# Optimization experiments

Hardware: AMD Instinct MI355X
Metric: run time of the kernel (lower is better)

Reference implementation:

```python
import jax, jax.numpy as jnp
import numpy as np

N_EMBD = 1024
N_HEAD = 16
HEAD_DIM = N_EMBD // N_HEAD


def setup_inputs() -> dict:
    key = jax.random.key(0)
    ks = jax.random.split(key, 9)
    B, T, C = 4, 2048, N_EMBD
    s = 1.0 / np.sqrt(C)
    return {
        "x": jax.random.normal(ks[0], (B, T, C), dtype=jnp.float32),
        "Wq": jax.random.normal(ks[1], (C, C), dtype=jnp.float32) * s,
        "bq": jnp.zeros((C,), dtype=jnp.float32),
        "Wk": jax.random.normal(ks[2], (C, C), dtype=jnp.float32) * s,
        "bk": jnp.zeros((C,), dtype=jnp.float32),
        "Wv": jax.random.normal(ks[3], (C, C), dtype=jnp.float32) * s,
        "bv": jnp.zeros((C,), dtype=jnp.float32),
        "Wo": jax.random.normal(ks[4], (C, C), dtype=jnp.float32) * s,
        "bo": jnp.zeros((C,), dtype=jnp.float32),
    }


def reference(x, Wq, bq, Wk, bk, Wv, bv, Wo, bo):
    B, T, C = x.shape
    H, D = N_HEAD, HEAD_DIM
    # torch Linear: y = x @ W.T + b ; here W stored as (in, out) so y = x @ W + b
    q = (x @ Wq + bq).reshape(B, T, H, D).transpose(0, 2, 1, 3)  # [B,H,T,D]
    k = (x @ Wk + bk).reshape(B, T, H, D).transpose(0, 2, 1, 3)
    v = (x @ Wv + bv).reshape(B, T, H, D).transpose(0, 2, 1, 3)
    scores = jnp.einsum('bhqd,bhkd->bhqk', q, k) / jnp.sqrt(jnp.float32(D))
    causal = jnp.tril(jnp.ones((T, T), dtype=bool))  # [T,T]
    scores = jnp.where(causal[None, None, :, :], scores, -jnp.inf)
    weights = jax.nn.softmax(scores, axis=-1)
    # dropout disabled (eval mode / deterministic reference)
    out = jnp.einsum('bhqk,bhkd->bhqd', weights, v)  # [B,H,T,D]
    out = out.transpose(0, 2, 1, 3).reshape(B, T, C)
    return out @ Wo + bo
```

## Files before the change

kernel.cpp:

```cpp
#include <hip/hip_runtime.h>
#include <stdint.h>
#include <stddef.h>

#define NB 4
#define NT 2048
#define NC 1024
#define NH 16
#define ND 64
#define NM (NB*NT)
#define KVB 64

typedef __bf16 bf16_t;
typedef __attribute__((ext_vector_type(8)))  __bf16 bf16x8;
typedef __attribute__((ext_vector_type(4)))  __bf16 bf16x4;
typedef __attribute__((ext_vector_type(2)))  __bf16 bf16x2;
typedef __attribute__((ext_vector_type(4)))  float  f32x4;
typedef __attribute__((ext_vector_type(16))) float  f32x16;
typedef __attribute__((ext_vector_type(4)))  unsigned int u32x4;

#define QK_SCALE_LOG2E 0.18033688011112042f

__device__ __forceinline__ f32x4 mfma_bf16(bf16x8 a, bf16x8 b, f32x4 c) {
  return __builtin_amdgcn_mfma_f32_16x16x32_bf16(a, b, c, 0, 0, 0);
}
__device__ __forceinline__ f32x16 mfma32(bf16x8 a, bf16x8 b, f32x16 c) {
  return __builtin_amdgcn_mfma_f32_32x32x16_bf16(a, b, c, 0, 0, 0);
}

__device__ __forceinline__ void gld_lds16(const void* g, void* l) {
  __builtin_amdgcn_global_load_lds(
      (const __attribute__((address_space(1))) void*)g,
      (__attribute__((address_space(3))) void*)l, 16, 0, 0);
}

__device__ __forceinline__ unsigned int pack_bf16(float a, float b) {
  bf16x2 t; t[0] = (bf16_t)a; t[1] = (bf16_t)b;
  return __builtin_bit_cast(unsigned int, t);
}

#if __has_builtin(__builtin_amdgcn_permlane32_swap)
typedef __attribute__((ext_vector_type(2))) unsigned int u32x2;
__device__ __forceinline__ void plswap(unsigned int &a, unsigned int &b) {
  u32x2 r = __builtin_amdgcn_permlane32_swap(a, b, false, false);
  a = r[0]; b = r[1];
}
#else
__device__ __forceinline__ void plswap(unsigned int &a, unsigned int &b) {
  asm volatile("s_nop 1\n\tv_permlane32_swap_b32 %0, %1\n\ts_nop 1"
               : "+v"(a), "+v"(b));
}
#endif

__global__ __launch_bounds__(256) void cast_x_kernel(const float* __restrict__ x,
                                                     bf16_t* __restrict__ xb, int n4) {
  const int stride = gridDim.x * blockDim.x;
  for (int i = blockIdx.x * blockDim.x + threadIdx.x; i < n4; i += stride) {
    float4 v = reinterpret_cast<const float4*>(x)[i];
    bf16x4 o;
    o[0] = (bf16_t)v.x; o[1] = (bf16_t)v.y; o[2] = (bf16_t)v.z; o[3] = (bf16_t)v.w;
    reinterpret_cast<bf16x4*>(xb)[i] = o;
  }
}

__global__ __launch_bounds__(256) void transpose_cast_kernel(const float* __restrict__ W,
                                                             bf16_t* __restrict__ WT) {
  __shared__ float tile[32][33];
  const int t = threadIdx.x;
  const int tx = t & 31, ty = t >> 5;
  const int k0 = (blockIdx.x & 31) << 5;
  const int n0 = (blockIdx.x >> 5) << 5;
#pragma unroll
  for (int i = 0; i < 4; ++i)
    tile[ty + 8*i][tx] = W[(size_t)(k0 + ty + 8*i)*NC + n0 + tx];
  __syncthreads();
#pragma unroll
  for (int i = 0; i < 4; ++i)
    WT[(size_t)(n0 + ty + 8*i)*NC + k0 + tx] = (bf16_t)tile[tx][ty + 8*i];
}

template<int MODE>
__global__ __launch_bounds__(256) void gemm_bt_kernel(
    const bf16_t* __restrict__ A, const bf16_t* __restrict__ BT,
    int M, int N, int K,
    bf16_t* __restrict__ qo, bf16_t* __restrict__ ko, bf16_t* __restrict__ vo,
    const float* __restrict__ b0, const float* __restrict__ b1, const float* __restrict__ b2,
    float* __restrict__ outp, const float* __restrict__ bo)
{
  const int lane = threadIdx.x & 63;
  const int wv = threadIdx.x >> 6;
  const int wr = wv >> 1, wc = wv & 1;
  const int l15 = lane & 15, lg = lane >> 4;
  const int nbn = N >> 7;
  const int bm = blockIdx.x / nbn, bn = blockIdx.x % nbn;
  const int m0 = bm << 7, n0 = bn << 7;

  __shared__ char smem[32768];
  char* As = smem;
  char* Bs = smem + 16384;

  f32x4 acc[4][4] = {};

  const int nkt = K >> 6;
  for (int kt = 0; kt < nkt; ++kt) {
    const int k0 = kt << 6;
    __syncthreads();
#pragma unroll
    for (int i = 0; i < 4; ++i) {
      const int seg = i*4 + wv;
      const int lin = seg*64 + lane;
      const int row = lin >> 3;
      const int ch  = (lin & 7) ^ (row & 7);
      gld_lds16(A  + (size_t)(m0 + row)*K + k0 + (ch << 3), As + seg*1024);
      gld_lds16(BT + (size_t)(n0 + row)*K + k0 + (ch << 3), Bs + seg*1024);
    }
    __syncthreads();
#pragma unroll
    for (int ks = 0; ks < 2; ++ks) {
      bf16x8 af[4], bfr[4];
#pragma unroll
      for (int fr = 0; fr < 4; ++fr) {
        const int row = wr*64 + fr*16 + l15;
        const int ch  = (ks*4 + lg) ^ (row & 7);
        af[fr] = *reinterpret_cast<const bf16x8*>(As + row*128 + ch*16);
      }
#pragma unroll
      for (int fc = 0; fc < 4; ++fc) {
        const int row = wc*64 + fc*16 + l15;
        const int ch  = (ks*4 + lg) ^ (row & 7);
        bfr[fc] = *reinterpret_cast<const bf16x8*>(Bs + row*128 + ch*16);
      }
#pragma unroll
      for (int fr = 0; fr < 4; ++fr)
#pragma unroll
        for (int fc = 0; fc < 4; ++fc)
          acc[fr][fc] = mfma_bf16(af[fr], bfr[fc], acc[fr][fc]);
    }
  }

#pragma unroll
  for (int fr = 0; fr < 4; ++fr) {
#pragma unroll
    for (int fc = 0; fc < 4; ++fc) {
      const int mrow0 = m0 + wr*64 + fr*16 + (lg << 2);
      const int ncol  = n0 + wc*64 + fc*16 + l15;
      if (MODE == 0) {
        const int mat = ncol >> 10, c = ncol & 1023;
        const int h = c >> 6, d = c & 63;
        if (mat == 2) {
          const float bias = b2[c];
          bf16x4 ov;
#pragma unroll
          for (int r = 0; r < 4; ++r) ov[r] = (bf16_t)(acc[fr][fc][r] + bias);
          const int bb = mrow0 >> 11, tt = mrow0 & (NT - 1);
          *reinterpret_cast<bf16x4*>(vo + ((((size_t)bb*NH + h)*ND + d)*NT) + tt) = ov;
        } else {
          bf16_t* dst = (mat == 0) ? qo : ko;
          const float* bptr = (mat == 0) ? b0 : b1;
          const float bias = bptr[c];
          const float scl = (mat == 0) ? QK_SCALE_LOG2E : 1.0f;
#pragma unroll
          for (int r = 0; r < 4; ++r) {
            const int mm = mrow0 + r;
            const int bb = mm >> 11, tt = mm & (NT - 1);
            dst[((((size_t)bb*NH + h)*NT + tt) << 6) + d] =
                (bf16_t)((acc[fr][fc][r] + bias) * scl);
          }
        }
      } else {
        const float bias = bo[ncol];
#pragma unroll
        for (int r = 0; r < 4; ++r)
          outp[(size_t)(mrow0 + r)*N + ncol] = acc[fr][fc][r] + bias;
      }
    }
  }
}

__global__ __launch_bounds__(512, 2) void attn_kernel(
    const bf16_t* __restrict__ q, const bf16_t* __restrict__ k, const bf16_t* __restrict__ vt,
    bf16_t* __restrict__ o)
{
  const int tid  = threadIdx.x;
  const int lane = tid & 63;
  const int wv   = tid >> 6;
  const int l31  = lane & 31, h = lane >> 5;

  const int tile = 7 - (blockIdx.x >> 6);
  const int bh   = blockIdx.x & 63;
  const int bb = bh >> 4, hh = bh & 15;
  const int q0 = tile << 8;

  __shared__ char smem[4*8192];
  char* const ks0 = smem;
  char* const ks1 = smem + 8192;
  char* const vs0 = smem + 16384;
  char* const vs1 = smem + 24576;

  const size_t base = (size_t)bh * (NT * ND);
  const bf16_t* Kg = k  + base;
  const bf16_t* Vg = vt + base;

  const int q0w = q0 + wv*32;
  const int qg  = q0w + l31;

  const int srow = tid >> 3;
  const int sch  = (tid & 7) ^ (srow & 7);
  const int offk = srow*ND + (sch << 3);
  const int offv = srow*NT + (sch << 3);
  const int segb = wv << 10;

  gld_lds16(Kg + offk, ks0 + segb);
  gld_lds16(Vg + offv, vs0 + segb);

  bf16x8 qf[4];
  {
    const bf16_t* Qg = q + base + (size_t)qg*ND + 8*h;
#pragma unroll
    for (int ds = 0; ds < 4; ++ds)
      qf[ds] = *reinterpret_cast<const bf16x8*>(Qg + 16*ds);
  }

  bf16x8 ones8;
#pragma unroll
  for (int jj = 0; jj < 8; ++jj) ones8[jj] = (bf16_t)1.0f;

  f32x16 oc[2] = {};
  f32x16 lacc = {};

  const int nkv = 4*(tile + 1);

  for (int j = 0; j < nkv; ++j) {
    const int kt0 = j << 6;
    const bool cur1 = (j & 1) != 0;
    char* const Kc = cur1 ? ks1 : ks0;
    char* const Vc = cur1 ? vs1 : vs0;

    asm volatile("s_waitcnt vmcnt(0)" ::: "memory");
    __builtin_amdgcn_s_barrier();
    __builtin_amdgcn_sched_barrier(0);

    if (j + 1 < nkv) {
      char* const Kn = cur1 ? ks0 : ks1;
      char* const Vn = cur1 ? vs0 : vs1;
      gld_lds16(Kg + (j + 1)*(KVB*ND) + offk, Kn + segb);
      gld_lds16(Vg + (j + 1)*KVB      + offv, Vn + segb);
      __builtin_amdgcn_sched_barrier(0);
    }

    if (kt0 <= q0w + 31) {
      f32x16 st[2] = {};
      __builtin_amdgcn_s_setprio(1);
#pragma unroll
      for (int ds = 0; ds < 4; ++ds) {
#pragma unroll
        for (int kt = 0; kt < 2; ++kt) {
          const int row = kt*32 + l31;
          const int cl  = (2*ds + h) ^ (row & 7);
          const bf16x8 kfr = *reinterpret_cast<const bf16x8*>(Kc + row*128 + cl*16);
          st[kt] = mfma32(kfr, qf[ds], st[kt]);
        }
      }
      __builtin_amdgcn_s_setprio(0);

      if (kt0 + KVB - 1 > q0w) {
        const int qrel = qg - kt0 - 4*h;
#pragma unroll
        for (int kt = 0; kt < 2; ++kt)
#pragma unroll
          for (int r = 0; r < 16; ++r) {
            const int kc = (r & 3) + 8*(r >> 2) + 32*kt;
            st[kt][r] = (kc > qrel) ? 0.0f : exp2f(st[kt][r]);
          }
      } else {
#pragma unroll
        for (int kt = 0; kt < 2; ++kt)
#pragma unroll
          for (int r = 0; r < 16; ++r)
            st[kt][r] = exp2f(st[kt][r]);
      }

#pragma unroll
      for (int kt = 0; kt < 2; ++kt) {
#pragma unroll
        for (int g = 0; g < 2; ++g) {
          unsigned int wa = pack_bf16(st[kt][8*g + 0], st[kt][8*g + 1]);
          unsigned int wb = pack_bf16(st[kt][8*g + 2], st[kt][8*g + 3]);
          unsigned int wc = pack_bf16(st[kt][8*g + 4], st[kt][8*g + 5]);
          unsigned int wd = pack_bf16(st[kt][8*g + 6], st[kt][8*g + 7]);
          plswap(wa, wc);
          plswap(wb, wd);
          u32x4 pb; pb[0] = wa; pb[1] = wb; pb[2] = wc; pb[3] = wd;
          const bf16x8 pf = __builtin_bit_cast(bf16x8, pb);
          const int kg = 2*kt + g;
          __builtin_amdgcn_s_setprio(1);
          lacc = mfma32(ones8, pf, lacc);
#pragma unroll
          for (int da = 0; da < 2; ++da) {
            const int row = 32*da + l31;
            const int cl  = (2*kg + h) ^ (row & 7);
            const bf16x8 vf = *reinterpret_cast<const bf16x8*>(Vc + row*128 + cl*16);
            oc[da] = mfma32(vf, pf, oc[da]);
          }
          __builtin_amdgcn_s_setprio(0);
        }
      }
    }
  }

  const float rl = 1.0f / lacc[0];
  bf16_t* orow = o + ((size_t)bb*NT + qg)*NC + hh*ND;
#pragma unroll
  for (int da = 0; da < 2; ++da) {
#pragma unroll
    for (int u = 0; u < 4; ++u) {
      bf16x4 ov;
#pragma unroll
      for (int jj = 0; jj < 4; ++jj) ov[jj] = (bf16_t)(oc[da][4*u + jj] * rl);
      *reinterpret_cast<bf16x4*>(orow + 32*da + 8*u + 4*h) = ov;
    }
  }
}

extern "C" void kernel_launch(void* const* d_in, const int* in_sizes, int n_in,
                              void* d_out, int out_size, void* d_ws, size_t ws_size,
                              hipStream_t stream) {
  (void)in_sizes; (void)n_in; (void)out_size;
  const float* x  = (const float*)d_in[0];
  const float* Wq = (const float*)d_in[1];
  const float* bq = (const float*)d_in[2];
  const float* Wk = (const float*)d_in[3];
  const float* bk = (const float*)d_in[4];
  const float* Wv = (const float*)d_in[5];
  const float* bv = (const float*)d_in[6];
  const float* Wo = (const float*)d_in[7];
  const float* bo = (const float*)d_in[8];
  float* out = (float*)d_out;

  const size_t off_xb    = 0;
  const size_t off_wqkvT = 16777216;
  const size_t off_woT   = 23068672;
  const size_t off_q     = 25165824;
  const size_t off_k     = 41943040;
  const size_t off_v     = 58720256;
  const size_t off_attn  = 75497472;
  const size_t need      = 92274688;
  if (ws_size < need) return;

  char* ws = (char*)d_ws;
  bf16_t* xb    = (bf16_t*)(ws + off_xb);
  bf16_t* wqkvT = (bf16_t*)(ws + off_wqkvT);
  bf16_t* woT   = (bf16_t*)(ws + off_woT);
  bf16_t* qb    = (bf16_t*)(ws + off_q);
  bf16_t* kb    = (bf16_t*)(ws + off_k);
  bf16_t* vtb   = (bf16_t*)(ws + off_v);
  bf16_t* attnb = (bf16_t*)(ws + off_attn);

  cast_x_kernel<<<dim3(2048), dim3(256), 0, stream>>>(x, xb, NM*NC/4);
  transpose_cast_kernel<<<dim3(1024), dim3(256), 0, stream>>>(Wq, wqkvT);
  transpose_cast_kernel<<<dim3(1024), dim3(256), 0, stream>>>(Wk, wqkvT + 1048576);
  transpose_cast_kernel<<<dim3(1024), dim3(256), 0, stream>>>(Wv, wqkvT + 2097152);
  transpose_cast_kernel<<<dim3(1024), dim3(256), 0, stream>>>(Wo, woT);

  gemm_bt_kernel<0><<<dim3(64*24), dim3(256), 0, stream>>>(
      xb, wqkvT, NM, 3*NC, NC, qb, kb, vtb, bq, bk, bv, nullptr, nullptr);

  attn_kernel<<<dim3(8*64), dim3(512), 0, stream>>>(qb, kb, vtb, attnb);

  gemm_bt_kernel<1><<<dim3(64*8), dim3(256), 0, stream>>>(
      attnb, woT, NM, NC, NC, nullptr, nullptr, nullptr, nullptr, nullptr, nullptr,
      out, bo);
}
```

Baseline: 178.8 us.

## Double attention KV tile to 128 and add separate V transpose kernel

The attention kernel now stages 128-key K/V tiles in a double-buffered 64KB LDS (wider V rows with a 16-way XOR swizzle) and processes each in two 64-key halves. This halves the barrier and prefetch iterations. The QKV GEMM writes V in row layout instead of with scattered transposed stores, and a new kernel transposes V into the reused x workspace. The four weight transpose launches are merged into one. The larger LDS footprint may cut occupancy under the two-blocks-per-CU launch bound, and the extra V transpose pass adds memory traffic.

```diff
diff --git a/kernel.cpp b/kernel.cpp
--- a/kernel.cpp
+++ b/kernel.cpp
@@ -8,7 +8,6 @@
 #define NH 16
 #define ND 64
 #define NM (NB*NT)
-#define KVB 64
 
 typedef __bf16 bf16_t;
 typedef __attribute__((ext_vector_type(8)))  __bf16 bf16x8;
@@ -62,13 +61,20 @@
   }
 }
 
-__global__ __launch_bounds__(256) void transpose_cast_kernel(const float* __restrict__ W,
-                                                             bf16_t* __restrict__ WT) {
+__global__ __launch_bounds__(256) void wtrans_kernel(
+    const float* __restrict__ Wq, const float* __restrict__ Wk,
+    const float* __restrict__ Wv, const float* __restrict__ Wo,
+    bf16_t* __restrict__ Tq, bf16_t* __restrict__ Tk,
+    bf16_t* __restrict__ Tv, bf16_t* __restrict__ To) {
   __shared__ float tile[32][33];
+  const int wsel = blockIdx.x >> 10;
+  const float* W = (wsel == 0) ? Wq : (wsel == 1) ? Wk : (wsel == 2) ? Wv : Wo;
+  bf16_t*     WT = (wsel == 0) ? Tq : (wsel == 1) ? Tk : (wsel == 2) ? Tv : To;
+  const int blk = blockIdx.x & 1023;
   const int t = threadIdx.x;
   const int tx = t & 31, ty = t >> 5;
-  const int k0 = (blockIdx.x & 31) << 5;
-  const int n0 = (blockIdx.x >> 5) << 5;
+  const int k0 = (blk & 31) << 5;
+  const int n0 = (blk >> 5) << 5;
 #pragma unroll
   for (int i = 0; i < 4; ++i)
     tile[ty + 8*i][tx] = W[(size_t)(k0 + ty + 8*i)*NC + n0 + tx];
@@ -76,6 +82,33 @@
 #pragma unroll
   for (int i = 0; i < 4; ++i)
     WT[(size_t)(n0 + ty + 8*i)*NC + k0 + tx] = (bf16_t)tile[tx][ty + 8*i];
+}
+
+__global__ __launch_bounds__(256) void vtrans_kernel(const bf16_t* __restrict__ v,
+                                                     bf16_t* __restrict__ vt) {
+  __shared__ bf16_t tile[64][72];
+  const int tid = threadIdx.x;
+  const int bh = blockIdx.x >> 5;
+  const int t0 = (blockIdx.x & 31) << 6;
+  const size_t base = (size_t)bh * (NT * ND);
+  {
+    const int r = tid >> 2, dc = (tid & 3) << 4;
+    const bf16_t* src = v + base + (size_t)(t0 + r)*ND + dc;
+    const bf16x8 a = *reinterpret_cast<const bf16x8*>(src);
+    const bf16x8 b = *reinterpret_cast<const bf16x8*>(src + 8);
+    *reinterpret_cast<bf16x8*>(&tile[r][dc])     = a;
+    *reinterpret_cast<bf16x8*>(&tile[r][dc + 8]) = b;
+  }
+  __syncthreads();
+  {
+    const int d = tid >> 2, tc = (tid & 3) << 4;
+    bf16x8 a, b;
+#pragma unroll
+    for (int i = 0; i < 8; ++i) { a[i] = tile[tc + i][d]; b[i] = tile[tc + 8 + i][d]; }
+    bf16_t* dst = vt + base + (size_t)d*NT + t0 + tc;
+    *reinterpret_cast<bf16x8*>(dst)     = a;
+    *reinterpret_cast<bf16x8*>(dst + 8) = b;
+  }
 }
 
 template<int MODE>
@@ -146,25 +179,16 @@
       if (MODE == 0) {
         const int mat = ncol >> 10, c = ncol & 1023;
         const int h = c >> 6, d = c & 63;
-        if (mat == 2) {
-          const float bias = b2[c];
-          bf16x4 ov;
-#pragma unroll
-          for (int r = 0; r < 4; ++r) ov[r] = (bf16_t)(acc[fr][fc][r] + bias);
-          const int bb = mrow0 >> 11, tt = mrow0 & (NT - 1);
-          *reinterpret_cast<bf16x4*>(vo + ((((size_t)bb*NH + h)*ND + d)*NT) + tt) = ov;
-        } else {
-          bf16_t* dst = (mat == 0) ? qo : ko;
-          const float* bptr = (mat == 0) ? b0 : b1;
-          const float bias = bptr[c];
-          const float scl = (mat == 0) ? QK_SCALE_LOG2E : 1.0f;
-#pragma unroll
-          for (int r = 0; r < 4; ++r) {
-            const int mm = mrow0 + r;
-            const int bb = mm >> 11, tt = mm & (NT - 1);
-            dst[((((size_t)bb*NH + h)*NT + tt) << 6) + d] =
-                (bf16_t)((acc[fr][fc][r] + bias) * scl);
-          }
+        bf16_t* dst = (mat == 0) ? qo : ((mat == 1) ? ko : vo);
+        const float* bptr = (mat == 0) ? b0 : ((mat == 1) ? b1 : b2);
+        const float bias = bptr[c];
+        const float scl = (mat == 0) ? QK_SCALE_LOG2E : 1.0f;
+#pragma unroll
+        for (int r = 0; r < 4; ++r) {
+          const int mm = mrow0 + r;
+          const int bb = mm >> 11, tt = mm & (NT - 1);
+          dst[((((size_t)bb*NH + h)*NT + tt) << 6) + d] =
+              (bf16_t)((acc[fr][fc][r] + bias) * scl);
         }
       } else {
         const float bias = bo[ncol];
@@ -190,11 +214,11 @@
   const int bb = bh >> 4, hh = bh & 15;
   const int q0 = tile << 8;
 
-  __shared__ char smem[4*8192];
+  __shared__ char smem[65536];
   char* const ks0 = smem;
-  char* const ks1 = smem + 8192;
-  char* const vs0 = smem + 16384;
-  char* const vs1 = smem + 24576;
+  char* const ks1 = smem + 16384;
+  char* const vs0 = smem + 32768;
+  char* const vs1 = smem + 49152;
 
   const size_t base = (size_t)bh * (NT * ND);
   const bf16_t* Kg = k  + base;
@@ -203,14 +227,24 @@
   const int q0w = q0 + wv*32;
   const int qg  = q0w + l31;
 
-  const int srow = tid >> 3;
-  const int sch  = (tid & 7) ^ (srow & 7);
-  const int offk = srow*ND + (sch << 3);
-  const int offv = srow*NT + (sch << 3);
-  const int segb = wv << 10;
-
-  gld_lds16(Kg + offk, ks0 + segb);
-  gld_lds16(Vg + offv, vs0 + segb);
+  int offk[2], offv[2], segb[2];
+#pragma unroll
+  for (int p = 0; p < 2; ++p) {
+    const int c = p*512 + tid;
+    const int krow = c >> 3;
+    const int kch  = (c & 7) ^ (krow & 7);
+    offk[p] = krow*ND + (kch << 3);
+    const int vrow = c >> 4;
+    const int vdc  = (c & 15) ^ (vrow & 15);
+    offv[p] = vrow*NT + (vdc << 3);
+    segb[p] = (p*8 + wv) << 10;
+  }
+
+#pragma unroll
+  for (int p = 0; p < 2; ++p) {
+    gld_lds16(Kg + offk[p], ks0 + segb[p]);
+    gld_lds16(Vg + offv[p], vs0 + segb[p]);
+  }
 
   bf16x8 qf[4];
   {
@@ -227,10 +261,9 @@
   f32x16 oc[2] = {};
   f32x16 lacc = {};
 
-  const int nkv = 4*(tile + 1);
+  const int nkv = 2*(tile + 1);
 
   for (int j = 0; j < nkv; ++j) {
-    const int kt0 = j << 6;
     const bool cur1 = (j & 1) != 0;
     char* const Kc = cur1 ? ks1 : ks0;
     char* const Vc = cur1 ? vs1 : vs0;
@@ -242,19 +275,29 @@
     if (j + 1 < nkv) {
       char* const Kn = cur1 ? ks0 : ks1;
       char* const Vn = cur1 ? vs0 : vs1;
-      gld_lds16(Kg + (j + 1)*(KVB*ND) + offk, Kn + segb);
-      gld_lds16(Vg + (j + 1)*KVB      + offv, Vn + segb);
+      const bf16_t* kp = Kg + (size_t)(j + 1)*(128*ND);
+      const bf16_t* vp = Vg + (size_t)(j + 1)*128;
+#pragma unroll
+      for (int p = 0; p < 2; ++p) {
+        gld_lds16(kp + offk[p], Kn + segb[p]);
+        gld_lds16(vp + offv[p], Vn + segb[p]);
+      }
       __builtin_amdgcn_sched_barrier(0);
     }
 
-    if (kt0 <= q0w + 31) {
+    const int ktile0 = j << 7;
+#pragma unroll 1
+    for (int hf = 0; hf < 2; ++hf) {
+      const int kb0 = ktile0 + (hf << 6);
+      if (kb0 > q0w + 31) break;
+
       f32x16 st[2] = {};
       __builtin_amdgcn_s_setprio(1);
 #pragma unroll
       for (int ds = 0; ds < 4; ++ds) {
 #pragma unroll
         for (int kt = 0; kt < 2; ++kt) {
-          const int row = kt*32 + l31;
+          const int row = (hf*2 + kt)*32 + l31;
           const int cl  = (2*ds + h) ^ (row & 7);
           const bf16x8 kfr = *reinterpret_cast<const bf16x8*>(Kc + row*128 + cl*16);
           st[kt] = mfma32(kfr, qf[ds], st[kt]);
@@ -262,8 +305,8 @@
       }
       __builtin_amdgcn_s_setprio(0);
 
-      if (kt0 + KVB - 1 > q0w) {
-        const int qrel = qg - kt0 - 4*h;
+      if (kb0 + 63 > q0w) {
+        const int qrel = qg - kb0 - 4*h;
 #pragma unroll
         for (int kt = 0; kt < 2; ++kt)
 #pragma unroll
@@ -291,14 +334,14 @@
           plswap(wb, wd);
           u32x4 pb; pb[0] = wa; pb[1] = wb; pb[2] = wc; pb[3] = wd;
           const bf16x8 pf = __builtin_bit_cast(bf16x8, pb);
-          const int kg = 2*kt + g;
+          const int cv = 2*(4*hf + 2*kt + g) + h;
           __builtin_amdgcn_s_setprio(1);
           lacc = mfma32(ones8, pf, lacc);
 #pragma unroll
           for (int da = 0; da < 2; ++da) {
             const int row = 32*da + l31;
-            const int cl  = (2*kg + h) ^ (row & 7);
-            const bf16x8 vf = *reinterpret_cast<const bf16x8*>(Vc + row*128 + cl*16);
+            const int lcv = cv ^ (row & 15);
+            const bf16x8 vf = *reinterpret_cast<const bf16x8*>(Vc + row*256 + lcv*16);
             oc[da] = mfma32(vf, pf, oc[da]);
           }
           __builtin_amdgcn_s_setprio(0);
@@ -352,17 +395,18 @@
   bf16_t* woT   = (bf16_t*)(ws + off_woT);
   bf16_t* qb    = (bf16_t*)(ws + off_q);
   bf16_t* kb    = (bf16_t*)(ws + off_k);
-  bf16_t* vtb   = (bf16_t*)(ws + off_v);
+  bf16_t* vb    = (bf16_t*)(ws + off_v);
+  bf16_t* vtb   = (bf16_t*)(ws + off_xb);
   bf16_t* attnb = (bf16_t*)(ws + off_attn);
 
   cast_x_kernel<<<dim3(2048), dim3(256), 0, stream>>>(x, xb, NM*NC/4);
-  transpose_cast_kernel<<<dim3(1024), dim3(256), 0, stream>>>(Wq, wqkvT);
-  transpose_cast_kernel<<<dim3(1024), dim3(256), 0, stream>>>(Wk, wqkvT + 1048576);
-  transpose_cast_kernel<<<dim3(1024), dim3(256), 0, stream>>>(Wv, wqkvT + 2097152);
-  transpose_cast_kernel<<<dim3(1024), dim3(256), 0, stream>>>(Wo, woT);
+  wtrans_kernel<<<dim3(4096), dim3(256), 0, stream>>>(
+      Wq, Wk, Wv, Wo, wqkvT, wqkvT + 1048576, wqkvT + 2097152, woT);
 
   gemm_bt_kernel<0><<<dim3(64*24), dim3(256), 0, stream>>>(
-      xb, wqkvT, NM, 3*NC, NC, qb, kb, vtb, bq, bk, bv, nullptr, nullptr);
+      xb, wqkvT, NM, 3*NC, NC, qb, kb, vb, bq, bk, bv, nullptr, nullptr);
+
+  vtrans_kernel<<<dim3(2048), dim3(256), 0, stream>>>(vb, vtb);
 
   attn_kernel<<<dim3(8*64), dim3(512), 0, stream>>>(qb, kb, vtb, attnb);
 
```

After: 178.6 us. Within noise of the previous version (-0.1%).
